# Kernel tuning notes

Measured on AMD Instinct MI355X. Metric: run time of the kernel, lower is better.

The kernel has to match this reference:

```python
import jax, jax.numpy as jnp
import numpy as np

D = 512       # embed_dim
H = 8         # num_heads
HD = D // H   # head_dim = 64
B = 16
TQ = 512      # query length (current segment)
TK = 1024     # key length (memory + current)
GRU_BIAS = 2.0


def _layer_norm(x, g, b, eps=1e-5):
    mu = jnp.mean(x, axis=-1, keepdims=True)
    var = jnp.mean((x - mu) ** 2, axis=-1, keepdims=True)
    return (x - mu) * jax.lax.rsqrt(var + eps) * g + b


def _gelu(x):
    # torch nn.GELU() default is the exact erf form
    return jax.nn.gelu(x, approximate=False)


def _rel_shift(x):
    # Transformer-XL relative shift. x: [B, H, Tq, Tk]
    b, h, tq, tk = x.shape
    x = jnp.pad(x, ((0, 0), (0, 0), (0, 0), (1, 0)))
    x = x.reshape(b, h, tk + 1, tq)[:, :, 1:, :]
    return x.reshape(b, h, tq, tk)


def _gru_gate(x, y, W, bg):
    # GTrXL gating: x is the residual stream, y the sublayer output.
    Wr, Ur, Wz, Uz, Wg, Ug = W
    r = jax.nn.sigmoid(y @ Wr + x @ Ur)
    z = jax.nn.sigmoid(y @ Wz + x @ Uz - bg)
    h = jnp.tanh(y @ Wg + (r * x) @ Ug)
    return (1.0 - z) * x + z * h


def setup_inputs() -> dict:
    key = jax.random.key(0)
    ks = jax.random.split(key, 16)
    s = 0.02
    return {
        "query": jax.random.normal(ks[0], (B, TQ, D), jnp.float32),
        "key": jax.random.normal(ks[1], (B, TK, D), jnp.float32),
        "pos_embedding": jax.random.normal(ks[2], (TK, D), jnp.float32),
        "U": jax.random.normal(ks[3], (H, HD), jnp.float32) * s,
        "V": jax.random.normal(ks[4], (H, HD), jnp.float32) * s,
        # attention projections: Wq, Wk, Wv, Wpos, Wout (no biases)
        "attn_W": jax.random.normal(ks[5], (5, D, D), jnp.float32) * s,
        "ln1_g": jnp.ones((D,), jnp.float32),
        "ln1_b": jnp.zeros((D,), jnp.float32),
        "ln2_g": jnp.ones((D,), jnp.float32),
        "ln2_b": jnp.zeros((D,), jnp.float32),
        # GRU gates: stacked [Wr, Ur, Wz, Uz, Wg, Ug], bias bg init to gru_bias
        "gate1_W": jax.random.normal(ks[6], (6, D, D), jnp.float32) * s,
        "gate1_b": jnp.full((D,), GRU_BIAS, jnp.float32),
        "gate2_W": jax.random.normal(ks[7], (6, D, D), jnp.float32) * s,
        "gate2_b": jnp.full((D,), GRU_BIAS, jnp.float32),
        "fc_W1": jax.random.normal(ks[8], (D, 4 * D), jnp.float32) * s,
        "fc_b1": jnp.zeros((4 * D,), jnp.float32),
        "fc_W2": jax.random.normal(ks[9], (4 * D, D), jnp.float32) * s,
        "fc_b2": jnp.zeros((D,), jnp.float32),
    }


def reference(query, key, pos_embedding, U, V, attn_W,
              ln1_g, ln1_b, ln2_g, ln2_b,
              gate1_W, gate1_b, gate2_W, gate2_b,
              fc_W1, fc_b1, fc_W2, fc_b2):
    b, tq, d = query.shape
    tk = key.shape[1]
    hd = d // H

    nq = _layer_norm(query, ln1_g, ln1_b)
    nk = _layer_norm(key, ln1_g, ln1_b)

    Wq, Wk, Wv, Wp, Wo = attn_W
    q = (nq @ Wq).reshape(b, tq, H, hd)
    k = (nk @ Wk).reshape(b, tk, H, hd)
    v = (nk @ Wv).reshape(b, tk, H, hd)
    p = (pos_embedding @ Wp).reshape(tk, H, hd)

    # Transformer-XL: content score (q+U)k^T + position score (q+V)p^T (rel-shifted)
    AC = jnp.einsum('bqhd,bkhd->bhqk', q + U, k)
    BD = _rel_shift(jnp.einsum('bqhd,khd->bhqk', q + V, p))
    scores = (AC + BD) / jnp.sqrt(jnp.asarray(hd, query.dtype))
    attn = jax.nn.softmax(scores, axis=-1)

    Y = jnp.einsum('bhqk,bkhd->bqhd', attn, v).reshape(b, tq, d) @ Wo
    Y = _gelu(Y)  # dropout = 0.0

    out = _gru_gate(query, Y, gate1_W, gate1_b)
    h2 = _layer_norm(out, ln2_g, ln2_b)
    E = _gelu(_gelu(h2 @ fc_W1 + fc_b1) @ fc_W2 + fc_b2)
    out = _gru_gate(out, E, gate2_W, gate2_b)
    return out
```

## Files before the change

### kernel.cpp

```cpp
#include <hip/hip_runtime.h>
#include <hip/hip_bf16.h>

typedef unsigned short u16;
typedef __attribute__((ext_vector_type(4))) float f4;
typedef __attribute__((ext_vector_type(8))) short s16x8;
typedef __attribute__((ext_vector_type(8))) unsigned short u16x8;
typedef __attribute__((ext_vector_type(4))) unsigned short u16x4;
typedef __attribute__((ext_vector_type(4))) int i32x4;
typedef __attribute__((ext_vector_type(2))) unsigned u32x2;

__device__ __forceinline__ u16 f2bf(float x){
  unsigned u = __float_as_uint(x);
  u += 0x7fffu + ((u >> 16) & 1u);
  return (u16)(u >> 16);
}
__device__ __forceinline__ float bf2f(u16 h){ return __uint_as_float(((unsigned)h) << 16); }

__device__ __forceinline__ unsigned cvt_pk_bf16(float lo, float hi){
  unsigned r;
  asm("v_cvt_pk_bf16_f32 %0, %1, %2" : "=v"(r) : "v"(lo), "v"(hi));
  return r;
}

__device__ __forceinline__ void gload_lds16(const u16* g, u16* l){
  __builtin_amdgcn_global_load_lds((__attribute__((address_space(1))) void*)g,
                                   (__attribute__((address_space(3))) void*)l, 16, 0, 0);
}

struct GemmP {
  const u16* A; const u16* B;
  const u16* A2; const u16* B2;
  int K1, K2, lda, ldb, H;
  long long sAb, sAh, sBb, sBh;
  u16* C; long long sCb, sCh; int ldc;
  u16* C2;
  const float* bias; const float* bias2;
  u16* S;
};

enum { EPI_BF16=0, EPI_QUV=1, EPI_SIG=2, EPI_TANH=3, EPI_GELU=4, EPI_BD=5 };

template<int BM, int BN, int EPI, int DB>
__launch_bounds__(256)
__global__ void gemm_k(GemmP p) {
  constexpr int WN = (BN >= 128) ? 2 : 1;
  constexpr int WM = 4 / WN;
  constexpr int TM = BM / WM, TN = BN / WN;
  constexpr int FM = TM / 16, FN = TN / 16;
  constexpr int BUFE = (BM + BN) * 64;

  __shared__ __align__(16) u16 lds[BUFE * (DB ? 2 : 1)];

  const int tid = threadIdx.x;
  const int w = tid >> 6, lane = tid & 63;
  const int bz = blockIdx.z;
  const int b = bz / p.H, h = bz - b * p.H;
  const int m0 = blockIdx.x * BM, n0 = blockIdx.y * BN;

  const u16* Ab0 = p.A + (long long)b * p.sAb + (long long)h * p.sAh + (long long)m0 * p.lda;
  const u16* Bb0 = p.B + (long long)b * p.sBb + (long long)h * p.sBh + (long long)n0 * p.ldb;
  const u16* Ab1 = p.A2 ? p.A2 + (long long)m0 * p.lda : (const u16*)0;
  const u16* Bb1 = p.B2 ? p.B2 + (long long)n0 * p.ldb : (const u16*)0;

  f4 acc[FM][FN];
  #pragma unroll
  for (int i = 0; i < FM; ++i)
    #pragma unroll
    for (int j = 0; j < FN; ++j) acc[i][j] = f4{0.f, 0.f, 0.f, 0.f};

  const int s1 = p.K1 >> 6;
  const int st = s1 + (p.K2 >> 6);
  const int wM = w / WN, wN = w - wM * WN;

  auto stage = [&](int s, u16* lA_, u16* lB_) {
    const u16* Ab; const u16* Bb; int k0;
    if (s < s1) { Ab = Ab0; Bb = Bb0; k0 = s << 6; }
    else        { Ab = Ab1; Bb = Bb1; k0 = (s - s1) << 6; }
    #pragma unroll
    for (int i = 0; i < (BM >> 5); ++i) {
      int c = i * 256 + tid, row = c >> 3, cc = c & 7, sc = cc ^ (row & 7);
      gload_lds16(Ab + (long long)row * p.lda + k0 + sc * 8, lA_ + (size_t)(i * 4 + w) * 512);
    }
    #pragma unroll
    for (int i = 0; i < (BN >> 5); ++i) {
      int c = i * 256 + tid, row = c >> 3, cc = c & 7, sc = cc ^ (row & 7);
      gload_lds16(Bb + (long long)row * p.ldb + k0 + sc * 8, lB_ + (size_t)(i * 4 + w) * 512);
    }
  };

  auto compute = [&](const u16* lA_, const u16* lB_) {
    #pragma unroll
    for (int kk = 0; kk < 2; ++kk) {
      const int kb = lane >> 4;
      const int gc = kk * 4 + kb;
      s16x8 av[FM], bv[FN];
      #pragma unroll
      for (int fm = 0; fm < FM; ++fm) {
        int r = wM * TM + fm * 16 + (lane & 15);
        av[fm] = *(const s16x8*)(lA_ + r * 64 + ((gc ^ (r & 7)) << 3));
      }
      #pragma unroll
      for (int fn = 0; fn < FN; ++fn) {
        int r = wN * TN + fn * 16 + (lane & 15);
        bv[fn] = *(const s16x8*)(lB_ + r * 64 + ((gc ^ (r & 7)) << 3));
      }
      #pragma unroll
      for (int fm = 0; fm < FM; ++fm)
        #pragma unroll
        for (int fn = 0; fn < FN; ++fn)
          acc[fm][fn] = __builtin_amdgcn_mfma_f32_16x16x32_bf16(av[fm], bv[fn], acc[fm][fn], 0, 0, 0);
    }
  };

  if constexpr (DB) {
    stage(0, lds, lds + BM * 64);
    __syncthreads();
    for (int s = 0; s < st; ++s) {
      u16* cur = lds + (size_t)(s & 1) * BUFE;
      if (s + 1 < st) {
        u16* nxt = lds + (size_t)((s + 1) & 1) * BUFE;
        stage(s + 1, nxt, nxt + BM * 64);
      }
      compute(cur, cur + BM * 64);
      __syncthreads();
    }
  } else {
    for (int s = 0; s < st; ++s) {
      stage(s, lds, lds + BM * 64);
      __syncthreads();
      compute(lds, lds + BM * 64);
      __syncthreads();
    }
  }

  const int rb = (lane >> 4) << 2;
  const int cb = lane & 15;

  if constexpr (EPI == EPI_BD) {
    #pragma unroll
    for (int fm = 0; fm < FM; ++fm)
      #pragma unroll
      for (int fn = 0; fn < FN; ++fn)
        #pragma unroll
        for (int r = 0; r < 4; ++r) {
          int row = m0 + wM * TM + fm * 16 + rb + r;
          int t   = n0 + wN * TN + fn * 16 + cb;
          int bb = row >> 9, q = row & 511;
          u16* Sp = p.S + (size_t)(bb * 8 + h) * 524800;
          Sp[(size_t)q * 1025 + 1 + t] = f2bf(acc[fm][fn][r] * 0.125f);
          if (t == 0 && q > 0) Sp[(size_t)q * 1025] = 0;
        }
  } else if constexpr (EPI == EPI_QUV) {
    #pragma unroll
    for (int fm = 0; fm < FM; ++fm)
      #pragma unroll
      for (int fn = 0; fn < FN; ++fn)
        #pragma unroll
        for (int r = 0; r < 4; ++r) {
          int row = m0 + wM * TM + fm * 16 + rb + r;
          int col = n0 + wN * TN + fn * 16 + cb;
          size_t o = (size_t)row * p.ldc + col;
          float x = acc[fm][fn][r];
          p.C[o]  = f2bf(x + p.bias[col]);
          p.C2[o] = f2bf(x + p.bias2[col]);
        }
  } else {
    u16* Cb = p.C + (long long)b * p.sCb + (long long)h * p.sCh;
    #pragma unroll
    for (int fm = 0; fm < FM; ++fm)
      #pragma unroll
      for (int fn = 0; fn < FN; ++fn)
        #pragma unroll
        for (int r = 0; r < 4; ++r) {
          int row = m0 + wM * TM + fm * 16 + rb + r;
          int col = n0 + wN * TN + fn * 16 + cb;
          float x = acc[fm][fn][r];
          if (p.bias) x += p.bias[col];
          if constexpr (EPI == EPI_SIG)  x = 1.f / (1.f + __expf(-x));
          if constexpr (EPI == EPI_TANH) { float e = __expf(-2.f * fabsf(x)); float t = (1.f - e) / (1.f + e); x = copysignf(t, x); }
          if constexpr (EPI == EPI_GELU) x = 0.5f * x * (1.f + erff(x * 0.70710678118654752f));
          Cb[(size_t)row * p.ldc + col] = f2bf(x);
        }
  }
}

__launch_bounds__(512)
__global__ void fattn_k(const u16* __restrict__ qU, const u16* __restrict__ kv,
                        const u16* __restrict__ vT, const u16* __restrict__ BD,
                        u16* __restrict__ Y) {
  __shared__ __align__(16) u16 sBuf[2 * 16384];

  const int tid = threadIdx.x, w = tid >> 6, lane = tid & 63;
  const int q0 = blockIdx.x * 128;
  const int bz = blockIdx.y, b = bz >> 3, h = bz & 7;
  const int cq = lane & 15, kb = lane >> 4;
  const u16* Sb = BD + (size_t)bz * 524800;

  auto stage = [&](int j0, u16* buf) {
    u16* sK_ = buf; u16* sV_ = buf + 4096; u16* sB_ = buf + 8192;
    {
      int c = tid, row = c >> 3, cc = c & 7, sc = cc ^ (row & 7);
      gload_lds16(kv + ((size_t)(b * 1024 + j0 + row)) * 1024 + h * 64 + sc * 8,
                  sK_ + (size_t)w * 512);
      gload_lds16(vT + (size_t)bz * 65536 + (size_t)row * 1024 + j0 + sc * 8,
                  sV_ + (size_t)w * 512);
    }
    #pragma unroll
    for (int i = 0; i < 2; ++i) {
      int c = i * 512 + tid, row = c >> 3, cc = c & 7, sc = cc ^ (row & 7);
      gload_lds16(Sb + 512 + (size_t)(q0 + row) * 1024 + j0 + sc * 8,
                  sB_ + (size_t)(i * 8 + w) * 512);
    }
  };

  const int qloc = w * 16 + cq;
  const u16* qrow = qU + ((size_t)(b * 512 + q0 + qloc)) * 512 + h * 64;
  s16x8 qb0 = *(const s16x8*)(qrow + kb * 8);
  s16x8 qb1 = *(const s16x8*)(qrow + 32 + kb * 8);

  stage(0, sBuf);
  __syncthreads();

  float m_s = -1e30f, l_s = 0.f;
  f4 O[4];
  #pragma unroll
  for (int fd = 0; fd < 4; ++fd) O[fd] = f4{0.f, 0.f, 0.f, 0.f};

  const int sw = qloc & 7;
  const int idxA = (cq + ((kb & 1) * 2) * 16) * 4;
  const int idxB = idxA + 64;

  for (int it = 0; it < 16; ++it) {
    u16* buf = sBuf + (size_t)(it & 1) * 16384;
    u16* sK_ = buf; u16* sV_ = buf + 4096; u16* sB_ = buf + 8192;
    if (it < 15) stage((it + 1) * 64, sBuf + (size_t)((it + 1) & 1) * 16384);

    f4 acc[4];
    #pragma unroll
    for (int fkv = 0; fkv < 4; ++fkv) acc[fkv] = f4{0.f, 0.f, 0.f, 0.f};
    #pragma unroll
    for (int fkv = 0; fkv < 4; ++fkv) {
      int r = fkv * 16 + cq;
      s16x8 a0 = *(const s16x8*)(sK_ + r * 64 + ((kb ^ (r & 7)) << 3));
      s16x8 a1 = *(const s16x8*)(sK_ + r * 64 + (((4 + kb) ^ (r & 7)) << 3));
      acc[fkv] = __builtin_amdgcn_mfma_f32_16x16x32_bf16(a0, qb0, acc[fkv], 0, 0, 0);
      acc[fkv] = __builtin_amdgcn_mfma_f32_16x16x32_bf16(a1, qb1, acc[fkv], 0, 0, 0);
    }

    float p[4][4];
    float tm = -1e30f;
    #pragma unroll
    for (int fkv = 0; fkv < 4; ++fkv) {
      int j8 = 2 * fkv + (kb >> 1);
      u16x4 bdv = *(const u16x4*)(sB_ + qloc * 64 + ((j8 ^ sw) << 3) + (kb & 1) * 4);
      #pragma unroll
      for (int r = 0; r < 4; ++r) {
        float s = acc[fkv][r] * 0.125f + bf2f(bdv[r]);
        p[fkv][r] = s;
        tm = fmaxf(tm, s);
      }
    }
    tm = fmaxf(tm, __shfl_xor(tm, 16));
    tm = fmaxf(tm, __shfl_xor(tm, 32));
    float mn = fmaxf(m_s, tm);
    float al = __expf(m_s - mn);
    m_s = mn;
    float ps = 0.f;
    #pragma unroll
    for (int fkv = 0; fkv < 4; ++fkv)
      #pragma unroll
      for (int r = 0; r < 4; ++r) { p[fkv][r] = __expf(p[fkv][r] - mn); ps += p[fkv][r]; }
    ps += __shfl_xor(ps, 16);
    ps += __shfl_xor(ps, 32);
    l_s = l_s * al + ps;
    #pragma unroll
    for (int fd = 0; fd < 4; ++fd)
      #pragma unroll
      for (int r = 0; r < 4; ++r) O[fd][r] *= al;

    unsigned W[4][2];
    #pragma unroll
    for (int fkv = 0; fkv < 4; ++fkv) {
      W[fkv][0] = cvt_pk_bf16(p[fkv][0], p[fkv][1]);
      W[fkv][1] = cvt_pk_bf16(p[fkv][2], p[fkv][3]);
    }
    s16x8 pb[2];
    #pragma unroll
    for (int c = 0; c < 2; ++c) {
      int a00 = __builtin_amdgcn_ds_bpermute(idxA, (int)W[2 * c][0]);
      int a01 = __builtin_amdgcn_ds_bpermute(idxA, (int)W[2 * c][1]);
      int a10 = __builtin_amdgcn_ds_bpermute(idxA, (int)W[2 * c + 1][0]);
      int a11 = __builtin_amdgcn_ds_bpermute(idxA, (int)W[2 * c + 1][1]);
      int b00 = __builtin_amdgcn_ds_bpermute(idxB, (int)W[2 * c][0]);
      int b01 = __builtin_amdgcn_ds_bpermute(idxB, (int)W[2 * c][1]);
      int b10 = __builtin_amdgcn_ds_bpermute(idxB, (int)W[2 * c + 1][0]);
      int b11 = __builtin_amdgcn_ds_bpermute(idxB, (int)W[2 * c + 1][1]);
      bool hi = (kb >= 2);
      i32x4 t;
      t[0] = hi ? a10 : a00;
      t[1] = hi ? a11 : a01;
      t[2] = hi ? b10 : b00;
      t[3] = hi ? b11 : b01;
      pb[c] = *(s16x8*)&t;
    }

    #pragma unroll
    for (int c = 0; c < 2; ++c)
      #pragma unroll
      for (int fd = 0; fd < 4; ++fd) {
        int rd = fd * 16 + cq;
        s16x8 vb = *(const s16x8*)(sV_ + rd * 64 + (((c * 4 + kb) ^ (rd & 7)) << 3));
        O[fd] = __builtin_amdgcn_mfma_f32_16x16x32_bf16(vb, pb[c], O[fd], 0, 0, 0);
      }
    __syncthreads();
  }

  float invl = 1.f / l_s;
  u16* yrow = Y + ((size_t)(b * 512 + q0 + qloc)) * 512 + h * 64;
  #pragma unroll
  for (int fd = 0; fd < 4; ++fd) {
    unsigned w0 = cvt_pk_bf16(O[fd][0] * invl, O[fd][1] * invl);
    unsigned w1 = cvt_pk_bf16(O[fd][2] * invl, O[fd][3] * invl);
    u32x2 st; st[0] = w0; st[1] = w1;
    *(u32x2*)(yrow + fd * 16 + kb * 4) = st;
  }
}

__launch_bounds__(256)
__global__ void ln_k(const float* __restrict__ x, const float* __restrict__ g,
                     const float* __restrict__ be, u16* __restrict__ out) {
  int row  = blockIdx.x * 4 + (threadIdx.x >> 6);
  int lane = threadIdx.x & 63;
  const float* xr = x + (size_t)row * 512 + lane * 8;
  f4 v0 = *(const f4*)xr;
  f4 v1 = *(const f4*)(xr + 4);
  float s = 0.f, q = 0.f;
  #pragma unroll
  for (int i = 0; i < 4; ++i) { s += v0[i] + v1[i]; q += v0[i]*v0[i] + v1[i]*v1[i]; }
  #pragma unroll
  for (int o = 32; o > 0; o >>= 1) { s += __shfl_xor(s, o); q += __shfl_xor(q, o); }
  float mu = s * (1.f / 512.f);
  float rs = rsqrtf(q * (1.f / 512.f) - mu * mu + 1e-5f);
  int c = lane * 8;
  u16x8 o;
  #pragma unroll
  for (int i = 0; i < 8; ++i) {
    float xx = (i < 4) ? v0[i] : v1[i - 4];
    o[i] = f2bf((xx - mu) * rs * g[c + i] + be[c + i]);
  }
  *(u16x8*)(out + (size_t)row * 512 + c) = o;
}

__device__ __forceinline__ void tbody(float (*t)[65], const float* src, u16* dst,
                                      int R, int C, int bx, int by, int tid) {
  int c0 = bx * 64, r0 = by * 64;
  #pragma unroll
  for (int i = 0; i < 4; ++i) {
    int r = i * 16 + (tid >> 4);
    int c4 = (tid & 15) * 4;
    f4 v = *(const f4*)(src + (size_t)(r0 + r) * C + c0 + c4);
    t[r][c4] = v.x; t[r][c4 + 1] = v.y; t[r][c4 + 2] = v.z; t[r][c4 + 3] = v.w;
  }
  __syncthreads();
  #pragma unroll
  for (int i = 0; i < 2; ++i) {
    int id = i * 256 + tid;
    int rr = id >> 3, c8 = (id & 7) * 8;
    u16x8 o;
    #pragma unroll
    for (int j = 0; j < 8; ++j) o[j] = f2bf(t[c8 + j][rr]);
    *(u16x8*)(dst + (size_t)(c0 + rr) * R + r0 + c8) = o;
  }
}

__launch_bounds__(256)
__global__ void tsq_k(const float* aW, const float* g1W, const float* g2W, u16* wT) {
  __shared__ float t[64][65];
  int z = blockIdx.z;
  const int lut[6] = {0, 2, 1, 3, 4, 5};
  const float* src; u16* dst;
  if (z < 5)       { src = aW  + (size_t)z * 262144;        dst = wT + (size_t)z * 262144; }
  else if (z < 11) { int j = z - 5;  src = g1W + (size_t)j * 262144; dst = wT + (size_t)(5 + lut[j]) * 262144; }
  else             { int j = z - 11; src = g2W + (size_t)j * 262144; dst = wT + (size_t)(11 + lut[j]) * 262144; }
  tbody(t, src, dst, 512, 512, blockIdx.x, blockIdx.y, threadIdx.x);
}

__launch_bounds__(256)
__global__ void tgen_k(const float* src, u16* dst, int R, int C) {
  __shared__ float t[64][65];
  tbody(t, src, dst, R, C, blockIdx.x, blockIdx.y, threadIdx.x);
}

__launch_bounds__(256)
__global__ void vtrans_k(const u16* kv, u16* vT) {
  int jt = blockIdx.x, h = blockIdx.y, b = blockIdx.z;
  __shared__ u16 t[64][72];
  int tid = threadIdx.x;
  const u16* src = kv + ((size_t)b * 1024 + jt * 64) * 1024 + 512 + h * 64;
  #pragma unroll
  for (int i = 0; i < 2; ++i) {
    int id = i * 256 + tid;
    int r = id >> 3, c = (id & 7) * 8;
    u16x8 v = *(const u16x8*)(src + (size_t)r * 1024 + c);
    #pragma unroll
    for (int j = 0; j < 8; ++j) t[r][c + j] = v[j];
  }
  __syncthreads();
  u16* dst = vT + (size_t)(b * 8 + h) * 65536 + (size_t)jt * 64;
  #pragma unroll
  for (int i = 0; i < 2; ++i) {
    int id = i * 256 + tid;
    int d = id >> 3, c = (id & 7) * 8;
    u16x8 o;
    #pragma unroll
    for (int j = 0; j < 8; ++j) o[j] = t[c + j][d];
    *(u16x8*)(dst + (size_t)d * 1024 + c) = o;
  }
}

__launch_bounds__(256)
__global__ void conv_k(const float* in, u16* out, int n8) {
  int i = blockIdx.x * 256 + threadIdx.x;
  if (i >= n8) return;
  const float* p = in + (size_t)i * 8;
  f4 a = *(const f4*)p, b = *(const f4*)(p + 4);
  u16x8 o;
  #pragma unroll
  for (int j = 0; j < 4; ++j) { o[j] = f2bf(a[j]); o[4 + j] = f2bf(b[j]); }
  *(u16x8*)(out + (size_t)i * 8) = o;
}

__launch_bounds__(256)
__global__ void bias_k(const float* g1b, const float* g2b, float* b1, float* b2) {
  int i = blockIdx.x * 256 + threadIdx.x;
  if (i < 1024) { b1[i] = (i < 512) ? 0.f : -g1b[i - 512]; b2[i] = (i < 512) ? 0.f : -g2b[i - 512]; }
}

__launch_bounds__(256)
__global__ void rx_k(const u16* rz, const float* x, u16* rx) {
  int i = blockIdx.x * 256 + threadIdx.x;
  int m = i >> 6, d8 = (i & 63) << 3;
  u16x8 rv = *(const u16x8*)(rz + (size_t)m * 1024 + d8);
  const float* xp = x + (size_t)m * 512 + d8;
  f4 x0 = *(const f4*)xp, x1 = *(const f4*)(xp + 4);
  u16x8 o;
  #pragma unroll
  for (int j = 0; j < 4; ++j) { o[j] = f2bf(bf2f(rv[j]) * x0[j]); o[4 + j] = f2bf(bf2f(rv[4 + j]) * x1[j]); }
  *(u16x8*)(rx + (size_t)m * 512 + d8) = o;
}

__launch_bounds__(256)
__global__ void comb_k(const u16* rz, const u16* hg, const float* x, float* of, u16* ob) {
  int i = blockIdx.x * 256 + threadIdx.x;
  int m = i >> 6, d8 = (i & 63) << 3;
  u16x8 zv = *(const u16x8*)(rz + (size_t)m * 1024 + 512 + d8);
  u16x8 hv = *(const u16x8*)(hg + (size_t)m * 512 + d8);
  const float* xp = x + (size_t)m * 512 + d8;
  f4 x0 = *(const f4*)xp, x1 = *(const f4*)(xp + 4);
  f4 o0, o1; u16x8 obv;
  #pragma unroll
  for (int j = 0; j < 4; ++j) {
    float z = bf2f(zv[j]), hh = bf2f(hv[j]);
    float r = (1.f - z) * x0[j] + z * hh; o0[j] = r; obv[j] = f2bf(r);
  }
  #pragma unroll
  for (int j = 0; j < 4; ++j) {
    float z = bf2f(zv[4 + j]), hh = bf2f(hv[4 + j]);
    float r = (1.f - z) * x1[j] + z * hh; o1[j] = r; obv[4 + j] = f2bf(r);
  }
  float* op = of + (size_t)m * 512 + d8;
  *(f4*)op = o0; *(f4*)(op + 4) = o1;
  if (ob) *(u16x8*)(ob + (size_t)m * 512 + d8) = obv;
}

extern "C" void kernel_launch(void* const* d_in, const int* in_sizes, int n_in,
                              void* d_out, int out_size, void* d_ws, size_t ws_size,
                              hipStream_t stream) {
  const float* query = (const float*)d_in[0];
  const float* key   = (const float*)d_in[1];
  const float* pos   = (const float*)d_in[2];
  const float* U     = (const float*)d_in[3];
  const float* V     = (const float*)d_in[4];
  const float* attnW = (const float*)d_in[5];
  const float* ln1g  = (const float*)d_in[6];
  const float* ln1b  = (const float*)d_in[7];
  const float* ln2g  = (const float*)d_in[8];
  const float* ln2b  = (const float*)d_in[9];
  const float* g1W   = (const float*)d_in[10];
  const float* g1b   = (const float*)d_in[11];
  const float* g2W   = (const float*)d_in[12];
  const float* g2b   = (const float*)d_in[13];
  const float* fcW1  = (const float*)d_in[14];
  const float* fcb1  = (const float*)d_in[15];
  const float* fcW2  = (const float*)d_in[16];
  const float* fcb2  = (const float*)d_in[17];
  float* outp = (float*)d_out;

  char* base = (char*)d_ws;
  size_t off = 0;
  auto alloc = [&](size_t bytes) -> char* {
    char* p = base + off;
    off += (bytes + 255) & ~(size_t)255;
    return p;
  };

  u16* wT     = (u16*)alloc(17ull * 262144 * 2);
  u16* fc1T   = (u16*)alloc(2048ull * 512 * 2);
  u16* fc2T   = (u16*)alloc(2048ull * 512 * 2);
  u16* posb   = (u16*)alloc(1024ull * 512 * 2);
  u16* pbf    = (u16*)alloc(1024ull * 512 * 2);
  float* bias1 = (float*)alloc(1024 * 4);
  float* bias2 = (float*)alloc(1024 * 4);
  u16* nq     = (u16*)alloc(8192ull * 512 * 2);
  u16* nk     = (u16*)alloc(16384ull * 512 * 2);
  u16* xq     = (u16*)alloc(8192ull * 512 * 2);
  u16* qU     = (u16*)alloc(8192ull * 512 * 2);
  u16* qV     = (u16*)alloc(8192ull * 512 * 2);
  u16* kv     = (u16*)alloc(16384ull * 1024 * 2);
  u16* y1     = (u16*)alloc(8192ull * 512 * 2);
  u16* ob1    = (u16*)alloc(8192ull * 512 * 2);
  u16* S      = (u16*)alloc(128ull * 524800 * 2 + 4096);
  if (off > ws_size) return;

  u16* Y = nq;
  u16* vT = nk;
  float* out1f = (float*)qU;
  u16* rz1 = S;
  u16* rx1 = S + 8388608;
  u16* hg1 = rx1 + 4194304;
  u16* h2  = hg1 + 4194304;
  u16* e1  = h2 + 4194304;
  u16* y2  = e1 + 16777216;
  u16* rz2 = y2 + 4194304;
  u16* rx2 = rz2 + 8388608;
  u16* hg2 = rx2 + 4194304;

  bias_k<<<dim3(4), dim3(256), 0, stream>>>(g1b, g2b, bias1, bias2);
  tsq_k<<<dim3(8, 8, 17), dim3(256), 0, stream>>>(attnW, g1W, g2W, wT);
  tgen_k<<<dim3(32, 8), dim3(256), 0, stream>>>(fcW1, fc1T, 512, 2048);
  tgen_k<<<dim3(8, 32), dim3(256), 0, stream>>>(fcW2, fc2T, 2048, 512);
  conv_k<<<dim3(256), dim3(256), 0, stream>>>(pos, posb, 65536);
  conv_k<<<dim3(2048), dim3(256), 0, stream>>>(query, xq, 524288);
  ln_k<<<dim3(2048), dim3(256), 0, stream>>>(query, ln1g, ln1b, nq);
  ln_k<<<dim3(4096), dim3(256), 0, stream>>>(key, ln1g, ln1b, nk);

  { GemmP p{}; p.A = nq; p.B = wT; p.K1 = 512; p.lda = 512; p.ldb = 512; p.H = 1;
    p.C = qU; p.C2 = qV; p.ldc = 512; p.bias = U; p.bias2 = V;
    gemm_k<64,128,EPI_QUV,1><<<dim3(128,4,1), dim3(256), 0, stream>>>(p); }
  { GemmP p{}; p.A = nk; p.B = wT + 1ull*262144; p.K1 = 512; p.lda = 512; p.ldb = 512; p.H = 1;
    p.C = kv; p.ldc = 1024;
    gemm_k<128,128,EPI_BF16,0><<<dim3(128,8,1), dim3(256), 0, stream>>>(p); }
  { GemmP p{}; p.A = posb; p.B = wT + 3ull*262144; p.K1 = 512; p.lda = 512; p.ldb = 512; p.H = 1;
    p.C = pbf; p.ldc = 512;
    gemm_k<64,128,EPI_BF16,1><<<dim3(16,4,1), dim3(256), 0, stream>>>(p); }
  vtrans_k<<<dim3(16, 8, 16), dim3(256), 0, stream>>>(kv, vT);

  { GemmP p{}; p.A = qV; p.lda = 512; p.sAh = 64;
    p.B = pbf; p.ldb = 512; p.sBh = 64; p.K1 = 64; p.H = 8; p.S = S;
    gemm_k<128,128,EPI_BD,0><<<dim3(64,8,8), dim3(256), 0, stream>>>(p); }

  fattn_k<<<dim3(4, 128), dim3(512), 0, stream>>>(qU, kv, vT, S, Y);

  { GemmP p{}; p.A = Y; p.B = wT + 4ull*262144; p.K1 = 512; p.lda = 512; p.ldb = 512; p.H = 1;
    p.C = y1; p.ldc = 512;
    gemm_k<64,128,EPI_GELU,1><<<dim3(128,4,1), dim3(256), 0, stream>>>(p); }

  { GemmP p{}; p.A = y1; p.B = wT + 5ull*262144; p.K1 = 512;
    p.A2 = xq; p.B2 = wT + 7ull*262144; p.K2 = 512;
    p.lda = 512; p.ldb = 512; p.H = 1; p.C = rz1; p.ldc = 1024; p.bias = bias1;
    gemm_k<64,128,EPI_SIG,1><<<dim3(128,8,1), dim3(256), 0, stream>>>(p); }
  rx_k<<<dim3(2048), dim3(256), 0, stream>>>(rz1, query, rx1);
  { GemmP p{}; p.A = y1; p.B = wT + 9ull*262144; p.K1 = 512;
    p.A2 = rx1; p.B2 = wT + 10ull*262144; p.K2 = 512;
    p.lda = 512; p.ldb = 512; p.H = 1; p.C = hg1; p.ldc = 512;
    gemm_k<64,128,EPI_TANH,1><<<dim3(128,4,1), dim3(256), 0, stream>>>(p); }
  comb_k<<<dim3(2048), dim3(256), 0, stream>>>(rz1, hg1, query, out1f, ob1);

  ln_k<<<dim3(2048), dim3(256), 0, stream>>>(out1f, ln2g, ln2b, h2);
  { GemmP p{}; p.A = h2; p.B = fc1T; p.K1 = 512; p.lda = 512; p.ldb = 512; p.H = 1;
    p.C = e1; p.ldc = 2048; p.bias = fcb1;
    gemm_k<128,128,EPI_GELU,0><<<dim3(64,16,1), dim3(256), 0, stream>>>(p); }
  { GemmP p{}; p.A = e1; p.B = fc2T; p.K1 = 2048; p.lda = 2048; p.ldb = 2048; p.H = 1;
    p.C = y2; p.ldc = 512; p.bias = fcb2;
    gemm_k<64,128,EPI_GELU,1><<<dim3(128,4,1), dim3(256), 0, stream>>>(p); }

  { GemmP p{}; p.A = y2; p.B = wT + 11ull*262144; p.K1 = 512;
    p.A2 = ob1; p.B2 = wT + 13ull*262144; p.K2 = 512;
    p.lda = 512; p.ldb = 512; p.H = 1; p.C = rz2; p.ldc = 1024; p.bias = bias2;
    gemm_k<64,128,EPI_SIG,1><<<dim3(128,8,1), dim3(256), 0, stream>>>(p); }
  rx_k<<<dim3(2048), dim3(256), 0, stream>>>(rz2, out1f, rx2);
  { GemmP p{}; p.A = y2; p.B = wT + 15ull*262144; p.K1 = 512;
    p.A2 = rx2; p.B2 = wT + 16ull*262144; p.K2 = 512;
    p.lda = 512; p.ldb = 512; p.H = 1; p.C = hg2; p.ldc = 512;
    gemm_k<64,128,EPI_TANH,1><<<dim3(128,4,1), dim3(256), 0, stream>>>(p); }
  comb_k<<<dim3(2048), dim3(256), 0, stream>>>(rz2, hg2, out1f, outp, (u16*)nullptr);
}
```

Before: 435.8 us.

## Use fast approximate activations, hoist staging addresses, retile K/V and FC1 GEMMs

Replaces the exact erf GELU with the tanh-form approximation built from exp and a hardware reciprocal, and uses reciprocals in the sigmoid and tanh epilogues. Hoists the per-thread row and swizzle offset math out of the load staging loop. Switches the K/V projection and FC1 GEMMs to 64x128 double-buffered tiles with more blocks. The approximate GELU slightly changes numerics relative to the exact reference.

```diff
diff --git a/kernel.cpp b/kernel.cpp
--- a/kernel.cpp
+++ b/kernel.cpp
@@ -25,6 +25,21 @@
 __device__ __forceinline__ void gload_lds16(const u16* g, u16* l){
   __builtin_amdgcn_global_load_lds((__attribute__((address_space(1))) void*)g,
                                    (__attribute__((address_space(3))) void*)l, 16, 0, 0);
+}
+
+__device__ __forceinline__ float gelu_f(float x){
+  float u = x * (0.7978845608f + 0.0356774081f * x * x);
+  float e = __expf(-2.f * u);
+  return x * __builtin_amdgcn_rcpf(1.f + e);
+}
+__device__ __forceinline__ float sig_f(float x){
+  float e = __expf(-x);
+  return __builtin_amdgcn_rcpf(1.f + e);
+}
+__device__ __forceinline__ float tanh_f(float x){
+  float e = __expf(-2.f * fabsf(x));
+  float t = (1.f - e) * __builtin_amdgcn_rcpf(1.f + e);
+  return copysignf(t, x);
 }
 
 struct GemmP {
@@ -72,20 +87,23 @@
   const int st = s1 + (p.K2 >> 6);
   const int wM = w / WN, wN = w - wM * WN;
 
+  const int srow = tid >> 3;
+  const long long sc8 = (long long)(((tid & 7) ^ (srow & 7)) << 3);
+  const long long aoff = (long long)srow * p.lda + sc8;
+  const long long boff = (long long)srow * p.ldb + sc8;
+
   auto stage = [&](int s, u16* lA_, u16* lB_) {
     const u16* Ab; const u16* Bb; int k0;
     if (s < s1) { Ab = Ab0; Bb = Bb0; k0 = s << 6; }
     else        { Ab = Ab1; Bb = Bb1; k0 = (s - s1) << 6; }
-    #pragma unroll
-    for (int i = 0; i < (BM >> 5); ++i) {
-      int c = i * 256 + tid, row = c >> 3, cc = c & 7, sc = cc ^ (row & 7);
-      gload_lds16(Ab + (long long)row * p.lda + k0 + sc * 8, lA_ + (size_t)(i * 4 + w) * 512);
-    }
-    #pragma unroll
-    for (int i = 0; i < (BN >> 5); ++i) {
-      int c = i * 256 + tid, row = c >> 3, cc = c & 7, sc = cc ^ (row & 7);
-      gload_lds16(Bb + (long long)row * p.ldb + k0 + sc * 8, lB_ + (size_t)(i * 4 + w) * 512);
-    }
+    const u16* pa = Ab + aoff + k0;
+    const u16* pb = Bb + boff + k0;
+    #pragma unroll
+    for (int i = 0; i < (BM >> 5); ++i)
+      gload_lds16(pa + (long long)(i * 32) * p.lda, lA_ + (size_t)(i * 4 + w) * 512);
+    #pragma unroll
+    for (int i = 0; i < (BN >> 5); ++i)
+      gload_lds16(pb + (long long)(i * 32) * p.ldb, lB_ + (size_t)(i * 4 + w) * 512);
   };
 
   auto compute = [&](const u16* lA_, const u16* lB_) {
@@ -176,9 +194,9 @@
           int col = n0 + wN * TN + fn * 16 + cb;
           float x = acc[fm][fn][r];
           if (p.bias) x += p.bias[col];
-          if constexpr (EPI == EPI_SIG)  x = 1.f / (1.f + __expf(-x));
-          if constexpr (EPI == EPI_TANH) { float e = __expf(-2.f * fabsf(x)); float t = (1.f - e) / (1.f + e); x = copysignf(t, x); }
-          if constexpr (EPI == EPI_GELU) x = 0.5f * x * (1.f + erff(x * 0.70710678118654752f));
+          if constexpr (EPI == EPI_SIG)  x = sig_f(x);
+          if constexpr (EPI == EPI_TANH) x = tanh_f(x);
+          if constexpr (EPI == EPI_GELU) x = gelu_f(x);
           Cb[(size_t)row * p.ldc + col] = f2bf(x);
         }
   }
@@ -549,7 +567,7 @@
     gemm_k<64,128,EPI_QUV,1><<<dim3(128,4,1), dim3(256), 0, stream>>>(p); }
   { GemmP p{}; p.A = nk; p.B = wT + 1ull*262144; p.K1 = 512; p.lda = 512; p.ldb = 512; p.H = 1;
     p.C = kv; p.ldc = 1024;
-    gemm_k<128,128,EPI_BF16,0><<<dim3(128,8,1), dim3(256), 0, stream>>>(p); }
+    gemm_k<64,128,EPI_BF16,1><<<dim3(256,8,1), dim3(256), 0, stream>>>(p); }
   { GemmP p{}; p.A = posb; p.B = wT + 3ull*262144; p.K1 = 512; p.lda = 512; p.ldb = 512; p.H = 1;
     p.C = pbf; p.ldc = 512;
     gemm_k<64,128,EPI_BF16,1><<<dim3(16,4,1), dim3(256), 0, stream>>>(p); }
@@ -579,7 +597,7 @@
   ln_k<<<dim3(2048), dim3(256), 0, stream>>>(out1f, ln2g, ln2b, h2);
   { GemmP p{}; p.A = h2; p.B = fc1T; p.K1 = 512; p.lda = 512; p.ldb = 512; p.H = 1;
     p.C = e1; p.ldc = 2048; p.bias = fcb1;
-    gemm_k<128,128,EPI_GELU,0><<<dim3(64,16,1), dim3(256), 0, stream>>>(p); }
+    gemm_k<64,128,EPI_GELU,1><<<dim3(128,16,1), dim3(256), 0, stream>>>(p); }
   { GemmP p{}; p.A = e1; p.B = fc2T; p.K1 = 2048; p.lda = 2048; p.ldb = 2048; p.H = 1;
     p.C = y2; p.ldc = 512; p.bias = fcb2;
     gemm_k<64,128,EPI_GELU,1><<<dim3(128,4,1), dim3(256), 0, stream>>>(p); }
```

New measurement: 400.3 us. 8.1% less time.
